# Kernel optimization log

Hardware: AMD Instinct MI355X
Metric: run time of the kernel (lower is better)

## Reference

```python
import jax, jax.numpy as jnp
import numpy as np

N = 100000
E = 1600000
H = 128
OUT = 16
NUM_GRAPHS = 64
BN_EPS = 1e-5


def setup_inputs() -> dict:
    key = jax.random.key(0)
    ks = jax.random.split(key, 16)
    x = jax.random.normal(ks[0], (N, 1), dtype=jnp.float32)
    edge_index = jax.random.randint(ks[1], (2, E), 0, N, dtype=jnp.int64)
    batch = jnp.sort(jax.random.randint(ks[2], (N,), 0, NUM_GRAPHS, dtype=jnp.int64))

    def glorot(k, shape):
        lim = float(np.sqrt(6.0 / (shape[0] + shape[1])))
        return jax.random.uniform(k, shape, jnp.float32, -lim, lim)

    return {
        "x": x, "edge_index": edge_index, "batch": batch,
        # conv 0: 1 -> H
        "W0": glorot(ks[3], (1, H)), "b0": jnp.zeros((H,), jnp.float32),
        "g0": jnp.ones((H,), jnp.float32), "beta0": jnp.zeros((H,), jnp.float32),
        # conv 1: H -> H
        "W1": glorot(ks[4], (H, H)), "b1": jnp.zeros((H,), jnp.float32),
        "g1": jnp.ones((H,), jnp.float32), "beta1": jnp.zeros((H,), jnp.float32),
        # conv 2: H -> H
        "W2": glorot(ks[5], (H, H)), "b2": jnp.zeros((H,), jnp.float32),
        "g2": jnp.ones((H,), jnp.float32), "beta2": jnp.zeros((H,), jnp.float32),
        # lin head
        "Wl": glorot(ks[6], (H, H)), "bl": jnp.zeros((H,), jnp.float32),
        "Wo": glorot(ks[7], (H, OUT)), "bo": jnp.zeros((OUT,), jnp.float32),
    }


def _gcn_norm(edge_index, n):
    # add self loops, symmetric normalization (PyG gcn_norm, edge_weight=1)
    loop = jnp.arange(n, dtype=edge_index.dtype)
    src = jnp.concatenate([edge_index[0], loop])
    dst = jnp.concatenate([edge_index[1], loop])
    deg = jax.ops.segment_sum(jnp.ones_like(src, jnp.float32), dst, num_segments=n)
    dis = jnp.where(deg > 0, jax.lax.rsqrt(deg), 0.0)
    return src, dst, dis[src] * dis[dst]


def _conv_bn_relu(h, src, dst, norm, n, W, b, g, beta):
    h = h @ W                                   # [N, H] linear transform first
    agg = jax.ops.segment_sum(h[src] * norm[:, None], dst, num_segments=n) + b
    m = agg.mean(axis=0)
    v = jnp.mean((agg - m) ** 2, axis=0)        # biased var (BN training mode)
    return jax.nn.relu(g * (agg - m) * jax.lax.rsqrt(v + BN_EPS) + beta)


def reference(x, edge_index, batch, W0, b0, g0, beta0, W1, b1, g1, beta1,
              W2, b2, g2, beta2, Wl, bl, Wo, bo):
    n = x.shape[0]
    src, dst, norm = _gcn_norm(edge_index, n)
    h = _conv_bn_relu(x, src, dst, norm, n, W0, b0, g0, beta0)
    h = _conv_bn_relu(h, src, dst, norm, n, W1, b1, g1, beta1)
    h = _conv_bn_relu(h, src, dst, norm, n, W2, b2, g2, beta2)
    # global mean pool per graph
    counts = jax.ops.segment_sum(jnp.ones((n,), h.dtype), batch, num_segments=NUM_GRAPHS)
    pooled = jax.ops.segment_sum(h, batch, num_segments=NUM_GRAPHS)
    pooled = pooled / jnp.maximum(counts, 1.0)[:, None]
    h = jax.nn.relu(pooled @ Wl + bl)
    return h @ Wo + bo
```

## Files before the change

kernel.cpp:

```cpp
#include <hip/hip_runtime.h>

#define HF 128
#define OUTF 16
#define NG 64
#define PBSH 7
#define PBSZ 128
#define CHUNK 4096
#define STAGE 4608
#define GBLK 2048
#define RBLK 128
#define BN_EPS 1e-5f

typedef unsigned short ushortT;
typedef unsigned int uintT;
typedef unsigned char ucharT;
typedef __attribute__((ext_vector_type(8))) short bf16x8;
typedef __attribute__((ext_vector_type(4))) float f32x4;
typedef __attribute__((ext_vector_type(2))) float f32x2;

__device__ __forceinline__ float bf2f(uintT u) {
    union { uintT i; float f; } c; c.i = u << 16; return c.f;
}
__device__ __forceinline__ float bf2f_hi(uintT u) {
    union { uintT i; float f; } c; c.i = u & 0xffff0000u; return c.f;
}
__device__ __forceinline__ uintT f2bf(float f) {
    union { float f; uintT i; } c; c.f = f;
    uintT u = c.i;
    return (u + 0x7fffu + ((u >> 16) & 1u)) >> 16;
}
__device__ __forceinline__ uintT pack2(float a, float b) {
    return f2bf(a) | (f2bf(b) << 16);
}

__device__ __forceinline__ uintT fp8_enc2(float a, float b) {
    return (uintT)__builtin_amdgcn_cvt_pk_fp8_f32(a, b, 0, false) & 0xffffu;
}
__device__ __forceinline__ void fp8_acc8(float* a, uint2 v) {
    f32x2 f;
    f = __builtin_amdgcn_cvt_pk_f32_fp8((int)v.x, false); a[0] += f.x; a[1] += f.y;
    f = __builtin_amdgcn_cvt_pk_f32_fp8((int)v.x, true);  a[2] += f.x; a[3] += f.y;
    f = __builtin_amdgcn_cvt_pk_f32_fp8((int)v.y, false); a[4] += f.x; a[5] += f.y;
    f = __builtin_amdgcn_cvt_pk_f32_fp8((int)v.y, true);  a[6] += f.x; a[7] += f.y;
}


__global__ __launch_bounds__(1024) void bhist_kernel(const int* __restrict__ dst,
                                                     int* __restrict__ bhistB,
                                                     int E, int nbkt) {
    __shared__ int h[1024];
    int t = threadIdx.x, blk = blockIdx.x;
    if (t < 1024) h[t] = 0;
    __syncthreads();
    int e0 = blk * CHUNK, e1 = min(E, e0 + CHUNK);
    for (int e = e0 + t; e < e1; e += 1024) atomicAdd(&h[dst[e] >> PBSH], 1);
    __syncthreads();
    if (t < nbkt) bhistB[blk * 1024 + t] = h[t];
}

__global__ __launch_bounds__(256) void bscan_blocks_kernel(const int* __restrict__ bhistB,
                                                           int* __restrict__ lbase,
                                                           int* __restrict__ total,
                                                           int nblk, int nbkt) {
    int bkt = blockIdx.x * 4 + (threadIdx.x >> 6);
    int lane = threadIdx.x & 63;
    if (bkt >= nbkt) return;
    int run = 0;
    for (int base = 0; base < nblk; base += 64) {
        int blk = base + lane;
        int v = (blk < nblk) ? bhistB[(size_t)blk * 1024 + bkt] : 0;
        int pre = v;
        #pragma unroll
        for (int o = 1; o < 64; o <<= 1) {
            int u = __shfl_up(pre, o);
            if (lane >= o) pre += u;
        }
        if (blk < nblk) lbase[(size_t)blk * 1024 + bkt] = run + pre - v;
        run += __shfl(pre, 63);
    }
    if (lane == 0) total[bkt] = run;
}

__global__ __launch_bounds__(1024) void bscan_base_kernel(const int* __restrict__ total,
                                                          int* __restrict__ bbase, int nbkt) {
    __shared__ int sc[1024];
    int t = threadIdx.x;
    int v = (t < nbkt) ? total[t] : 0;
    sc[t] = v;
    __syncthreads();
    for (int o = 1; o < 1024; o <<= 1) {
        int add = (t >= o) ? sc[t - o] : 0;
        __syncthreads();
        sc[t] += add;
        __syncthreads();
    }
    if (t < nbkt) {
        bbase[t] = sc[t] - v;
        if (t == nbkt - 1) bbase[nbkt] = sc[t];
    }
}

__global__ __launch_bounds__(1024) void bscatter_kernel(const int* __restrict__ src,
                                                        const int* __restrict__ dst,
                                                        const int* __restrict__ bbase,
                                                        const int* __restrict__ lbase,
                                                        uintT* __restrict__ tmp,
                                                        int E, int nbkt) {
    __shared__ int cur[1024];
    int t = threadIdx.x, blk = blockIdx.x;
    if (t < nbkt) cur[t] = bbase[t] + lbase[(size_t)blk * 1024 + t];
    __syncthreads();
    int e0 = blk * CHUNK, e1 = min(E, e0 + CHUNK);
    for (int e = e0 + t; e < e1; e += 1024) {
        int d = dst[e];
        int bkt = d >> PBSH;
        int pos = atomicAdd(&cur[bkt], 1);
        tmp[pos] = ((uintT)(d & (PBSZ - 1)) << 18) | (uintT)src[e];
    }
}

__global__ __launch_bounds__(256) void breorder_kernel(const uintT* __restrict__ tmp,
                                                       const int* __restrict__ bbase,
                                                       const float* __restrict__ x,
                                                       int* __restrict__ rowptr,
                                                       int* __restrict__ csr_src,
                                                       float* __restrict__ dis,
                                                       float* __restrict__ xp,
                                                       int n, int nbkt) {
    __shared__ int lcnt[PBSZ];
    __shared__ int sc[PBSZ];
    __shared__ int lcur[PBSZ];
    __shared__ int stage[STAGE];
    int b = blockIdx.x, t = threadIdx.x;
    int n0 = b << PBSH;
    if (n0 >= n) return;
    int start = bbase[b], end = bbase[b + 1];
    int cnt = end - start;
    if (t < PBSZ) lcnt[t] = 0;
    __syncthreads();
    for (int i = t; i < cnt; i += 256) atomicAdd(&lcnt[tmp[start + i] >> 18], 1);
    __syncthreads();
    int v = (t < PBSZ) ? lcnt[t] : 0;
    if (t < PBSZ) sc[t] = v;
    __syncthreads();
    for (int o = 1; o < PBSZ; o <<= 1) {
        int add = (t < PBSZ && t >= o) ? sc[t - o] : 0;
        __syncthreads();
        if (t < PBSZ) sc[t] += add;
        __syncthreads();
    }
    if (t < PBSZ) {
        int pre = sc[t] - v;
        lcur[t] = pre;
        int node = n0 + t;
        if (node < n) {
            rowptr[node] = start + pre;
            float d = rsqrtf((float)v + 1.0f);
            dis[node] = d;
            xp[node] = d * x[node];
        }
    }
    if (b == nbkt - 1 && t == 0) rowptr[n] = end;
    __syncthreads();
    if (cnt <= STAGE) {
        for (int i = t; i < cnt; i += 256) {
            uintT p = tmp[start + i];
            int pos = atomicAdd(&lcur[p >> 18], 1);
            stage[pos] = (int)(p & 0x3ffffu);
        }
        __syncthreads();
        for (int i = t; i < cnt; i += 256) csr_src[start + i] = stage[i];
    } else {
        for (int i = t; i < cnt; i += 256) {
            uintT p = tmp[start + i];
            int pos = atomicAdd(&lcur[p >> 18], 1);
            csr_src[start + pos] = (int)(p & 0x3ffffu);
        }
    }
}


__global__ __launch_bounds__(256) void gather1_kernel(const float* __restrict__ xp,
                                                      const int* __restrict__ rowptr,
                                                      const int* __restrict__ csr_src,
                                                      const float* __restrict__ dis,
                                                      float* __restrict__ aggx,
                                                      float* __restrict__ partial1, int n) {
    int t = threadIdx.x;
    int i = blockIdx.x * 256 + t;
    float v = 0.f;
    if (i < n) {
        float acc = xp[i];
        int e = rowptr[i + 1];
        for (int j = rowptr[i]; j < e; ++j) acc += xp[csr_src[j]];
        v = acc * dis[i];
        aggx[i] = v;
    }
    float s = v, ss = v * v;
    for (int o = 32; o > 0; o >>= 1) { s += __shfl_down(s, o); ss += __shfl_down(ss, o); }
    __shared__ float r2[2][4];
    int wv = t >> 6, ln = t & 63;
    if (ln == 0) { r2[0][wv] = s; r2[1][wv] = ss; }
    __syncthreads();
    if (t == 0) {
        partial1[blockIdx.x * 2]     = r2[0][0] + r2[0][1] + r2[0][2] + r2[0][3];
        partial1[blockIdx.x * 2 + 1] = r2[1][0] + r2[1][1] + r2[1][2] + r2[1][3];
    }
}

__global__ void coef0_kernel(const float* __restrict__ partial1, int nblk1,
                             const float* __restrict__ W0, const float* __restrict__ g,
                             const float* __restrict__ beta, float* __restrict__ coef,
                             float invn) {
    __shared__ float rs[128], rss[128];
    int t = threadIdx.x;
    float s = 0.f, ss = 0.f;
    for (int k = t; k < nblk1; k += 128) { s += partial1[2 * k]; ss += partial1[2 * k + 1]; }
    rs[t] = s; rss[t] = ss;
    __syncthreads();
    for (int o = 64; o > 0; o >>= 1) {
        if (t < o) { rs[t] += rs[t + o]; rss[t] += rss[t + o]; }
        __syncthreads();
    }
    float m = rs[0] * invn;
    float var = rss[0] * invn - m * m;
    float w = W0[t];
    float sc = g[t] * w * rsqrtf(var * w * w + BN_EPS);
    coef[t] = sc;
    coef[HF + t] = beta[t] - m * sc;
}


__global__ void wprep2_kernel(const float* __restrict__ W1, const float* __restrict__ W2,
                              ushortT* __restrict__ Wt1, ushortT* __restrict__ Wt2) {
    int i = blockIdx.x * 256 + threadIdx.x;
    const float* W = (i < 16384) ? W1 : W2;
    ushortT* Wt = (i < 16384) ? Wt1 : Wt2;
    int ii = i & 16383;
    int k = ii >> 7, j = ii & 127;
    int byteoff = (j << 8) + ((k << 1) ^ ((j & 7) << 4));
    *(ushortT*)((char*)Wt + byteoff) = (ushortT)f2bf(W[ii]);
}


__global__ __launch_bounds__(256) void gemm_mfma_kernel(const ushortT* __restrict__ A,
                                                        const float* __restrict__ aggx,
                                                        const ushortT* __restrict__ Wt8,
                                                        const float* __restrict__ coef,
                                                        const float* __restrict__ dis,
                                                        ucharT* __restrict__ C8, int n,
                                                        int mode) {
    __shared__ uint4 Wt[2048];
    int t = threadIdx.x;
    int wave = t >> 6, lane = t & 63;
    int l4 = lane >> 4;
    int lm = lane & 15;

    {
        const uint4* ws = reinterpret_cast<const uint4*>(Wt8);
        #pragma unroll
        for (int i = 0; i < 8; ++i) Wt[t + i * 256] = ws[t + i * 256];
    }
    __syncthreads();

    int rowBase = blockIdx.x * 64 + wave * 16;
    int ar = rowBase + lm;
    int arc = min(ar, n - 1);

    bf16x8 af[4];
    if (mode == 2) {
        float a = aggx[arc];
        #pragma unroll
        for (int kb = 0; kb < 4; ++kb) {
            int k0 = kb * 32 + l4 * 8;
            float4 sc0 = *reinterpret_cast<const float4*>(coef + k0);
            float4 sc1 = *reinterpret_cast<const float4*>(coef + k0 + 4);
            float4 sh0 = *reinterpret_cast<const float4*>(coef + HF + k0);
            float4 sh1 = *reinterpret_cast<const float4*>(coef + HF + k0 + 4);
            float scv[8] = {sc0.x, sc0.y, sc0.z, sc0.w, sc1.x, sc1.y, sc1.z, sc1.w};
            float shv[8] = {sh0.x, sh0.y, sh0.z, sh0.w, sh1.x, sh1.y, sh1.z, sh1.w};
            bf16x8 o;
            #pragma unroll
            for (int j = 0; j < 8; ++j) {
                float f = fmaxf(a * scv[j] + shv[j], 0.f);
                o[j] = (short)f2bf(f);
            }
            af[kb] = o;
        }
    } else {
        #pragma unroll
        for (int kb = 0; kb < 4; ++kb) {
            int k0 = kb * 32 + l4 * 8;
            bf16x8 v = *reinterpret_cast<const bf16x8*>(A + (size_t)arc * HF + k0);
            if (mode == 1) {
                float4 sc0 = *reinterpret_cast<const float4*>(coef + k0);
                float4 sc1 = *reinterpret_cast<const float4*>(coef + k0 + 4);
                float4 sh0 = *reinterpret_cast<const float4*>(coef + HF + k0);
                float4 sh1 = *reinterpret_cast<const float4*>(coef + HF + k0 + 4);
                float scv[8] = {sc0.x, sc0.y, sc0.z, sc0.w, sc1.x, sc1.y, sc1.z, sc1.w};
                float shv[8] = {sh0.x, sh0.y, sh0.z, sh0.w, sh1.x, sh1.y, sh1.z, sh1.w};
                bf16x8 o;
                #pragma unroll
                for (int j = 0; j < 8; ++j) {
                    float f = bf2f((uintT)(ushortT)v[j]);
                    f = fmaxf(f * scv[j] + shv[j], 0.f);
                    o[j] = (short)f2bf(f);
                }
                v = o;
            }
            af[kb] = v;
        }
    }

    f32x4 acc[8];
    #pragma unroll
    for (int ct = 0; ct < 8; ++ct) acc[ct] = (f32x4){0.f, 0.f, 0.f, 0.f};

    #pragma unroll
    for (int ct = 0; ct < 8; ++ct) {
        int col = ct * 16 + lm;
        int rowbyte = col << 8;
        int swz = (col & 7) << 4;
        #pragma unroll
        for (int kb = 0; kb < 4; ++kb) {
            int off = ((kb * 64 + l4 * 16) ^ swz);
            bf16x8 bf = *reinterpret_cast<const bf16x8*>((const char*)Wt + rowbyte + off);
            acc[ct] = __builtin_amdgcn_mfma_f32_16x16x32_bf16(af[kb], bf, acc[ct], 0, 0, 0);
        }
    }

    int rbase = rowBase + l4 * 4;
    float4 d4;
    if (rbase <= n - 4) {
        d4 = *reinterpret_cast<const float4*>(dis + rbase);
    } else {
        float tmp4[4];
        #pragma unroll
        for (int r = 0; r < 4; ++r) tmp4[r] = (rbase + r < n) ? dis[rbase + r] : 0.f;
        d4 = make_float4(tmp4[0], tmp4[1], tmp4[2], tmp4[3]);
    }
    const float* dd = (const float*)&d4;
    #pragma unroll
    for (int ct = 0; ct < 8; ++ct) {
        #pragma unroll
        for (int r = 0; r < 4; ++r) {
            float v = acc[ct][r] * dd[r];
            float o = __shfl_xor(v, 1);
            uintT pk = fp8_enc2(v, o);
            pk |= __shfl_xor(pk, 2) << 16;
            int row = rbase + r;
            if ((lane & 3) == 0 && row < n) {
                *(uintT*)(C8 + (size_t)row * HF + ct * 16 + lm) = pk;
            }
        }
    }
}


__global__ __launch_bounds__(256) void gather_stats_kernel(const ucharT* __restrict__ h8,
                                                           const int* __restrict__ rowptr,
                                                           const int* __restrict__ csr_src,
                                                           const float* __restrict__ dis,
                                                           ushortT* __restrict__ agg,
                                                           float* __restrict__ partial,
                                                           int n) {
    __shared__ float part[4][256];
    int t = threadIdx.x;
    int wave = t >> 6, lane = t & 63;
    int grp = lane >> 4;
    int l = lane & 15;
    float s[8], ss[8];
    #pragma unroll
    for (int i = 0; i < 8; ++i) { s[i] = 0.f; ss[i] = 0.f; }

    for (int node = blockIdx.x * 4 + wave; node < n; node += GBLK * 4) {
        int beg = rowptr[node], end = rowptr[node + 1];
        float a[8];
        #pragma unroll
        for (int i = 0; i < 8; ++i) a[i] = 0.f;
        if (grp == 0) {
            uint2 v = *reinterpret_cast<const uint2*>(h8 + (size_t)node * HF + l * 8);
            fp8_acc8(a, v);
        }
        for (int base = beg; base < end; base += 64) {
            int idx = base + lane;
            int sj = (idx < end) ? csr_src[idx] : 0;
            int cnt = min(64, end - base);
            for (int j = 0; j < cnt; j += 4) {
                int e = j + grp;
                int srcn = __shfl(sj, e < 64 ? e : 63);
                if (e < cnt) {
                    uint2 v = *reinterpret_cast<const uint2*>(h8 + (size_t)srcn * HF + l * 8);
                    fp8_acc8(a, v);
                }
            }
        }
        #pragma unroll
        for (int i = 0; i < 8; ++i) {
            a[i] += __shfl_xor(a[i], 16);
            a[i] += __shfl_xor(a[i], 32);
        }
        if (grp == 0) {
            float dd = dis[node];
            #pragma unroll
            for (int i = 0; i < 8; ++i) {
                a[i] *= dd;
                s[i] += a[i];
                ss[i] += a[i] * a[i];
            }
            uint4 o;
            o.x = pack2(a[0], a[1]);
            o.y = pack2(a[2], a[3]);
            o.z = pack2(a[4], a[5]);
            o.w = pack2(a[6], a[7]);
            *reinterpret_cast<uint4*>(agg + (size_t)node * HF + l * 8) = o;
        }
    }

    if (grp == 0) {
        #pragma unroll
        for (int i = 0; i < 8; ++i) {
            part[wave][l * 8 + i] = s[i];
            part[wave][128 + l * 8 + i] = ss[i];
        }
    }
    __syncthreads();
    float v = part[0][t] + part[1][t] + part[2][t] + part[3][t];
    partial[(size_t)blockIdx.x * 256 + t] = v;
}

__global__ __launch_bounds__(256) void reduce128_kernel(const float* __restrict__ partial,
                                                        float* __restrict__ partial2, int nblk) {
    int t = threadIdx.x, b = blockIdx.x;
    float acc = 0.f;
    for (int r = b; r < nblk; r += RBLK) acc += partial[(size_t)r * 256 + t];
    partial2[b * 256 + t] = acc;
}

__global__ void bn_coef_kernel(const float* __restrict__ partial2, const float* __restrict__ g,
                               const float* __restrict__ beta, float* __restrict__ coef,
                               float invn) {
    __shared__ float st[256];
    int t = threadIdx.x;
    float a = 0.f;
    #pragma unroll 8
    for (int b = 0; b < RBLK; ++b) a += partial2[b * 256 + t];
    st[t] = a;
    __syncthreads();
    if (t < 128) {
        float m = st[t] * invn;
        float v = st[128 + t] * invn - m * m;
        float sc = g[t] * rsqrtf(v + BN_EPS);
        coef[t] = sc;
        coef[HF + t] = beta[t] - m * sc;
    }
}


__global__ void starts_kernel(const int* __restrict__ batch, int* __restrict__ starts,
                              float* __restrict__ pooled, int n) {
    int g = threadIdx.x;
    if (g <= NG) {
        int lo = 0, hi = n;
        while (lo < hi) {
            int mid = (lo + hi) >> 1;
            if (batch[mid] < g) lo = mid + 1; else hi = mid;
        }
        starts[g] = lo;
    }
    for (int i = threadIdx.x; i < NG * HF; i += 128) pooled[i] = 0.f;
}

__global__ void pool_kernel(const ushortT* __restrict__ h, const float* __restrict__ coef,
                            const int* __restrict__ starts, float* __restrict__ pooled) {
    int g = blockIdx.x >> 4;
    int p = blockIdx.x & 15;
    int lane = threadIdx.x;
    float sc0 = coef[lane * 2],     sc1 = coef[lane * 2 + 1];
    float sh0 = coef[HF + lane * 2], sh1 = coef[HF + lane * 2 + 1];
    int s = starts[g], e = starts[g + 1];
    int len = e - s;
    int chunk = (len + 15) >> 4;
    int r0 = s + p * chunk;
    int r1 = min(e, r0 + chunk);
    float a0 = 0.f, a1 = 0.f;
    for (int r = r0; r < r1; ++r) {
        uintT v = *reinterpret_cast<const uintT*>(h + (size_t)r * HF + lane * 2);
        a0 += fmaxf(bf2f(v & 0xffff) * sc0 + sh0, 0.f);
        a1 += fmaxf(bf2f_hi(v) * sc1 + sh1, 0.f);
    }
    if (r1 > r0) {
        atomicAdd(&pooled[g * HF + lane * 2], a0);
        atomicAdd(&pooled[g * HF + lane * 2 + 1], a1);
    }
}


__global__ __launch_bounds__(1024) void head_kernel(const float* __restrict__ pooled,
                                                    const int* __restrict__ starts,
                                                    const float* __restrict__ Wl,
                                                    const float* __restrict__ bl,
                                                    const float* __restrict__ Wo,
                                                    const float* __restrict__ bo,
                                                    float* __restrict__ out) {
    __shared__ float P[NG][HF];
    __shared__ float T[NG][HF];
    int t = threadIdx.x;
    for (int i = t; i < NG * HF; i += 1024) {
        int g = i >> 7;
        float cnt = fmaxf((float)(starts[g + 1] - starts[g]), 1.0f);
        P[g][i & 127] = pooled[i] / cnt;
    }
    __syncthreads();
    for (int i = t; i < NG * HF; i += 1024) {
        int g = i >> 7, j = i & 127;
        float acc = bl[j];
        for (int k = 0; k < HF; ++k) acc += P[g][k] * Wl[k * HF + j];
        T[g][j] = fmaxf(acc, 0.f);
    }
    __syncthreads();
    int g = t >> 4, o = t & 15;
    float acc = bo[o];
    for (int k = 0; k < HF; ++k) acc += T[g][k] * Wo[k * OUTF + o];
    out[t] = acc;
}


extern "C" void kernel_launch(void* const* d_in, const int* in_sizes, int n_in,
                              void* d_out, int out_size, void* d_ws, size_t ws_size,
                              hipStream_t stream) {
    const float* x     = (const float*)d_in[0];
    const int*   ei    = (const int*)d_in[1];
    const int*   batch = (const int*)d_in[2];
    const float* W0 = (const float*)d_in[3];
    const float* g0 = (const float*)d_in[5];
    const float* be0 = (const float*)d_in[6];
    const float* W1 = (const float*)d_in[7];
    const float* g1 = (const float*)d_in[9];
    const float* be1 = (const float*)d_in[10];
    const float* W2 = (const float*)d_in[11];
    const float* g2 = (const float*)d_in[13];
    const float* be2 = (const float*)d_in[14];
    const float* Wl = (const float*)d_in[15];
    const float* bl = (const float*)d_in[16];
    const float* Wo = (const float*)d_in[17];
    const float* bo = (const float*)d_in[18];

    const int n = in_sizes[0];
    const int E = in_sizes[1] / 2;
    const int* srcI = ei;
    const int* dstI = ei + E;
    const int nbkt = (n + PBSZ - 1) >> PBSH;
    const int nblk = (E + CHUNK - 1) / CHUNK;
    const int nblk1 = (n + 255) / 256;

    ushortT* bufA = (ushortT*)d_ws;
    ushortT* bufB = bufA + (size_t)n * HF;
    ucharT* bufB8 = (ucharT*)bufB;
    float* dis    = (float*)(bufB + (size_t)n * HF);
    float* xp     = dis + n;
    float* aggx   = xp + n;
    float* coef   = aggx + n;
    float* pooled = coef + 2 * HF;
    int* rowptr   = (int*)(pooled + NG * HF);
    int* csr_src  = rowptr + n + 1;
    uintT* tmp    = (uintT*)(csr_src + E);
    int* bhistB   = (int*)(tmp + E);
    int* lbase    = bhistB + (size_t)nblk * 1024;
    int* total    = lbase + (size_t)nblk * 1024;
    int* bbase    = total + 1024;
    int* starts   = bbase + 1025;
    float* partial = (float*)(starts + NG + 1);
    float* partial2 = partial + (size_t)GBLK * 256;
    float* partial1 = partial2 + RBLK * 256;
    ushortT* wbuf1 = (ushortT*)(partial1 + (size_t)nblk1 * 2 + 2);
    ushortT* wbuf2 = wbuf1 + 16384;

    bhist_kernel<<<nblk, 1024, 0, stream>>>(dstI, bhistB, E, nbkt);
    bscan_blocks_kernel<<<(nbkt + 3) / 4, 256, 0, stream>>>(bhistB, lbase, total, nblk, nbkt);
    bscan_base_kernel<<<1, 1024, 0, stream>>>(total, bbase, nbkt);
    bscatter_kernel<<<nblk, 1024, 0, stream>>>(srcI, dstI, bbase, lbase, tmp, E, nbkt);
    breorder_kernel<<<nbkt, 256, 0, stream>>>(tmp, bbase, x, rowptr, csr_src, dis, xp, n, nbkt);

    gather1_kernel<<<nblk1, 256, 0, stream>>>(xp, rowptr, csr_src, dis, aggx, partial1, n);
    coef0_kernel<<<1, 128, 0, stream>>>(partial1, nblk1, W0, g0, be0, coef, 1.0f / n);

    wprep2_kernel<<<128, 256, 0, stream>>>(W1, W2, wbuf1, wbuf2);

    gemm_mfma_kernel<<<(n + 63) / 64, 256, 0, stream>>>(bufA, aggx, wbuf1, coef, dis, bufB8, n, 2);
    gather_stats_kernel<<<GBLK, 256, 0, stream>>>(bufB8, rowptr, csr_src, dis, bufA, partial, n);
    reduce128_kernel<<<RBLK, 256, 0, stream>>>(partial, partial2, GBLK);
    bn_coef_kernel<<<1, 256, 0, stream>>>(partial2, g1, be1, coef, 1.0f / n);

    gemm_mfma_kernel<<<(n + 63) / 64, 256, 0, stream>>>(bufA, aggx, wbuf2, coef, dis, bufB8, n, 1);
    gather_stats_kernel<<<GBLK, 256, 0, stream>>>(bufB8, rowptr, csr_src, dis, bufA, partial, n);
    reduce128_kernel<<<RBLK, 256, 0, stream>>>(partial, partial2, GBLK);
    bn_coef_kernel<<<1, 256, 0, stream>>>(partial2, g2, be2, coef, 1.0f / n);

    starts_kernel<<<1, 128, 0, stream>>>(batch, starts, pooled, n);
    pool_kernel<<<NG * 16, 64, 0, stream>>>(bufA, coef, starts, pooled);
    head_kernel<<<1, 1024, 0, stream>>>(pooled, starts, Wl, bl, Wo, bo, (float*)d_out);
}
```

Baseline: 300.3 us.

## Slice feature buffers into 16-column planes and gather one node per thread

```diff
diff --git a/kernel.cpp b/kernel.cpp
--- a/kernel.cpp
+++ b/kernel.cpp
@@ -3,11 +3,12 @@
 #define HF 128
 #define OUTF 16
 #define NG 64
+#define NSL 8
+#define SLC 16
 #define PBSH 7
 #define PBSZ 128
 #define CHUNK 4096
 #define STAGE 4608
-#define GBLK 2048
 #define RBLK 128
 #define BN_EPS 1e-5f
 
@@ -42,6 +43,10 @@
     f = __builtin_amdgcn_cvt_pk_f32_fp8((int)v.x, true);  a[2] += f.x; a[3] += f.y;
     f = __builtin_amdgcn_cvt_pk_f32_fp8((int)v.y, false); a[4] += f.x; a[5] += f.y;
     f = __builtin_amdgcn_cvt_pk_f32_fp8((int)v.y, true);  a[6] += f.x; a[7] += f.y;
+}
+__device__ __forceinline__ void fp8_acc16(float* a, uint4 v) {
+    fp8_acc8(a,     make_uint2(v.x, v.y));
+    fp8_acc8(a + 8, make_uint2(v.z, v.w));
 }
 
 
@@ -291,8 +296,9 @@
         #pragma unroll
         for (int kb = 0; kb < 4; ++kb) {
             int k0 = kb * 32 + l4 * 8;
-            bf16x8 v = *reinterpret_cast<const bf16x8*>(A + (size_t)arc * HF + k0);
-            if (mode == 1) {
+            const ushortT* ap = A + ((size_t)(k0 >> 4) * n + arc) * SLC + (k0 & 15);
+            bf16x8 v = *reinterpret_cast<const bf16x8*>(ap);
+            {
                 float4 sc0 = *reinterpret_cast<const float4*>(coef + k0);
                 float4 sc1 = *reinterpret_cast<const float4*>(coef + k0 + 4);
                 float4 sh0 = *reinterpret_cast<const float4*>(coef + HF + k0);
@@ -350,90 +356,74 @@
             pk |= __shfl_xor(pk, 2) << 16;
             int row = rbase + r;
             if ((lane & 3) == 0 && row < n) {
-                *(uintT*)(C8 + (size_t)row * HF + ct * 16 + lm) = pk;
+                *(uintT*)(C8 + ((size_t)ct * n + row) * SLC + lm) = pk;
             }
         }
     }
 }
 
 
-__global__ __launch_bounds__(256) void gather_stats_kernel(const ucharT* __restrict__ h8,
+__global__ __launch_bounds__(256) void gather_stats_kernel(const ucharT* __restrict__ h8T,
                                                            const int* __restrict__ rowptr,
                                                            const int* __restrict__ csr_src,
                                                            const float* __restrict__ dis,
-                                                           ushortT* __restrict__ agg,
+                                                           ushortT* __restrict__ aggT,
                                                            float* __restrict__ partial,
                                                            int n) {
-    __shared__ float part[4][256];
-    int t = threadIdx.x;
-    int wave = t >> 6, lane = t & 63;
-    int grp = lane >> 4;
-    int l = lane & 15;
-    float s[8], ss[8];
+    int t = threadIdx.x;
+    int s = blockIdx.x & 7;
+    int node = (blockIdx.x >> 3) * 256 + t;
+    const ucharT* base = h8T + (size_t)s * n * SLC;
+
+    float a[16];
     #pragma unroll
-    for (int i = 0; i < 8; ++i) { s[i] = 0.f; ss[i] = 0.f; }
-
-    for (int node = blockIdx.x * 4 + wave; node < n; node += GBLK * 4) {
+    for (int i = 0; i < 16; ++i) a[i] = 0.f;
+
+    if (node < n) {
+        uint4 v = *reinterpret_cast<const uint4*>(base + (size_t)node * SLC);
+        fp8_acc16(a, v);
         int beg = rowptr[node], end = rowptr[node + 1];
-        float a[8];
-        #pragma unroll
-        for (int i = 0; i < 8; ++i) a[i] = 0.f;
-        if (grp == 0) {
-            uint2 v = *reinterpret_cast<const uint2*>(h8 + (size_t)node * HF + l * 8);
-            fp8_acc8(a, v);
-        }
-        for (int base = beg; base < end; base += 64) {
-            int idx = base + lane;
-            int sj = (idx < end) ? csr_src[idx] : 0;
-            int cnt = min(64, end - base);
-            for (int j = 0; j < cnt; j += 4) {
-                int e = j + grp;
-                int srcn = __shfl(sj, e < 64 ? e : 63);
-                if (e < cnt) {
-                    uint2 v = *reinterpret_cast<const uint2*>(h8 + (size_t)srcn * HF + l * 8);
-                    fp8_acc8(a, v);
-                }
-            }
-        }
-        #pragma unroll
-        for (int i = 0; i < 8; ++i) {
-            a[i] += __shfl_xor(a[i], 16);
-            a[i] += __shfl_xor(a[i], 32);
-        }
-        if (grp == 0) {
-            float dd = dis[node];
-            #pragma unroll
-            for (int i = 0; i < 8; ++i) {
-                a[i] *= dd;
-                s[i] += a[i];
-                ss[i] += a[i] * a[i];
-            }
-            uint4 o;
-            o.x = pack2(a[0], a[1]);
-            o.y = pack2(a[2], a[3]);
-            o.z = pack2(a[4], a[5]);
-            o.w = pack2(a[6], a[7]);
-            *reinterpret_cast<uint4*>(agg + (size_t)node * HF + l * 8) = o;
-        }
-    }
-
-    if (grp == 0) {
-        #pragma unroll
-        for (int i = 0; i < 8; ++i) {
-            part[wave][l * 8 + i] = s[i];
-            part[wave][128 + l * 8 + i] = ss[i];
-        }
-    }
-    __syncthreads();
-    float v = part[0][t] + part[1][t] + part[2][t] + part[3][t];
-    partial[(size_t)blockIdx.x * 256 + t] = v;
+        for (int j = beg; j < end; ++j) {
+            int srcn = csr_src[j];
+            uint4 w = *reinterpret_cast<const uint4*>(base + (size_t)srcn * SLC);
+            fp8_acc16(a, w);
+        }
+        float dd = dis[node];
+        #pragma unroll
+        for (int i = 0; i < 16; ++i) a[i] *= dd;
+        uint4 o1, o2;
+        o1.x = pack2(a[0], a[1]);   o1.y = pack2(a[2], a[3]);
+        o1.z = pack2(a[4], a[5]);   o1.w = pack2(a[6], a[7]);
+        o2.x = pack2(a[8], a[9]);   o2.y = pack2(a[10], a[11]);
+        o2.z = pack2(a[12], a[13]); o2.w = pack2(a[14], a[15]);
+        uint4* dst = reinterpret_cast<uint4*>(aggT + ((size_t)s * n + node) * SLC);
+        dst[0] = o1; dst[1] = o2;
+    }
+
+    __shared__ float red[4][32];
+    int wv = t >> 6, ln = t & 63;
+    #pragma unroll
+    for (int i = 0; i < 16; ++i) {
+        float si = a[i], qi = a[i] * a[i];
+        for (int o = 32; o > 0; o >>= 1) {
+            si += __shfl_down(si, o);
+            qi += __shfl_down(qi, o);
+        }
+        if (ln == 0) { red[wv][i] = si; red[wv][16 + i] = qi; }
+    }
+    __syncthreads();
+    if (t < 32) {
+        partial[(size_t)blockIdx.x * 32 + t] =
+            red[0][t] + red[1][t] + red[2][t] + red[3][t];
+    }
 }
 
 __global__ __launch_bounds__(256) void reduce128_kernel(const float* __restrict__ partial,
-                                                        float* __restrict__ partial2, int nblk) {
+                                                        float* __restrict__ partial2, int ngrp) {
     int t = threadIdx.x, b = blockIdx.x;
+    int s = t >> 5, o = t & 31;
     float acc = 0.f;
-    for (int r = b; r < nblk; r += RBLK) acc += partial[(size_t)r * 256 + t];
+    for (int j = b; j < ngrp; j += RBLK) acc += partial[(size_t)(j * 8 + s) * 32 + o];
     partial2[b * 256 + t] = acc;
 }
 
@@ -448,8 +438,9 @@
     st[t] = a;
     __syncthreads();
     if (t < 128) {
-        float m = st[t] * invn;
-        float v = st[128 + t] * invn - m * m;
+        int sl = t >> 4, c = t & 15;
+        float m = st[sl * 32 + c] * invn;
+        float v = st[sl * 32 + 16 + c] * invn - m * m;
         float sc = g[t] * rsqrtf(v + BN_EPS);
         coef[t] = sc;
         coef[HF + t] = beta[t] - m * sc;
@@ -471,12 +462,15 @@
     for (int i = threadIdx.x; i < NG * HF; i += 128) pooled[i] = 0.f;
 }
 
-__global__ void pool_kernel(const ushortT* __restrict__ h, const float* __restrict__ coef,
-                            const int* __restrict__ starts, float* __restrict__ pooled) {
+__global__ void pool_kernel(const ushortT* __restrict__ hT, const float* __restrict__ coef,
+                            const int* __restrict__ starts, float* __restrict__ pooled, int n) {
     int g = blockIdx.x >> 4;
     int p = blockIdx.x & 15;
     int lane = threadIdx.x;
-    float sc0 = coef[lane * 2],     sc1 = coef[lane * 2 + 1];
+    int sl = lane >> 3;
+    int ci = (lane * 2) & 15;
+    const ushortT* hp = hT + (size_t)sl * n * SLC + ci;
+    float sc0 = coef[lane * 2],      sc1 = coef[lane * 2 + 1];
     float sh0 = coef[HF + lane * 2], sh1 = coef[HF + lane * 2 + 1];
     int s = starts[g], e = starts[g + 1];
     int len = e - s;
@@ -485,7 +479,7 @@
     int r1 = min(e, r0 + chunk);
     float a0 = 0.f, a1 = 0.f;
     for (int r = r0; r < r1; ++r) {
-        uintT v = *reinterpret_cast<const uintT*>(h + (size_t)r * HF + lane * 2);
+        uintT v = *reinterpret_cast<const uintT*>(hp + (size_t)r * SLC);
         a0 += fmaxf(bf2f(v & 0xffff) * sc0 + sh0, 0.f);
         a1 += fmaxf(bf2f_hi(v) * sc1 + sh1, 0.f);
     }
@@ -553,6 +547,7 @@
     const int nbkt = (n + PBSZ - 1) >> PBSH;
     const int nblk = (E + CHUNK - 1) / CHUNK;
     const int nblk1 = (n + 255) / 256;
+    const int ngrp = (n + 255) / 256;
 
     ushortT* bufA = (ushortT*)d_ws;
     ushortT* bufB = bufA + (size_t)n * HF;
@@ -571,7 +566,7 @@
     int* bbase    = total + 1024;
     int* starts   = bbase + 1025;
     float* partial = (float*)(starts + NG + 1);
-    float* partial2 = partial + (size_t)GBLK * 256;
+    float* partial2 = partial + (size_t)ngrp * 8 * 32;
     float* partial1 = partial2 + RBLK * 256;
     ushortT* wbuf1 = (ushortT*)(partial1 + (size_t)nblk1 * 2 + 2);
     ushortT* wbuf2 = wbuf1 + 16384;
@@ -588,16 +583,16 @@
     wprep2_kernel<<<128, 256, 0, stream>>>(W1, W2, wbuf1, wbuf2);
 
     gemm_mfma_kernel<<<(n + 63) / 64, 256, 0, stream>>>(bufA, aggx, wbuf1, coef, dis, bufB8, n, 2);
-    gather_stats_kernel<<<GBLK, 256, 0, stream>>>(bufB8, rowptr, csr_src, dis, bufA, partial, n);
-    reduce128_kernel<<<RBLK, 256, 0, stream>>>(partial, partial2, GBLK);
+    gather_stats_kernel<<<ngrp * 8, 256, 0, stream>>>(bufB8, rowptr, csr_src, dis, bufA, partial, n);
+    reduce128_kernel<<<RBLK, 256, 0, stream>>>(partial, partial2, ngrp);
     bn_coef_kernel<<<1, 256, 0, stream>>>(partial2, g1, be1, coef, 1.0f / n);
 
     gemm_mfma_kernel<<<(n + 63) / 64, 256, 0, stream>>>(bufA, aggx, wbuf2, coef, dis, bufB8, n, 1);
-    gather_stats_kernel<<<GBLK, 256, 0, stream>>>(bufB8, rowptr, csr_src, dis, bufA, partial, n);
-    reduce128_kernel<<<RBLK, 256, 0, stream>>>(partial, partial2, GBLK);
+    gather_stats_kernel<<<ngrp * 8, 256, 0, stream>>>(bufB8, rowptr, csr_src, dis, bufA, partial, n);
+    reduce128_kernel<<<RBLK, 256, 0, stream>>>(partial, partial2, ngrp);
     bn_coef_kernel<<<1, 256, 0, stream>>>(partial2, g2, be2, coef, 1.0f / n);
 
     starts_kernel<<<1, 128, 0, stream>>>(batch, starts, pooled, n);
-    pool_kernel<<<NG * 16, 64, 0, stream>>>(bufA, coef, starts, pooled);
+    pool_kernel<<<NG * 16, 64, 0, stream>>>(bufA, coef, starts, pooled, n);
     head_kernel<<<1, 1024, 0, stream>>>(pooled, starts, Wl, bl, Wo, bo, (float*)d_out);
 }
```

Result: slower. 438.3 us (+45.9%).
